# Kernel tuning notes

Hardware: AMD Instinct MI355X
Metric: run time of the kernel (lower is better)

Reference implementation:

```python
import jax, jax.numpy as jnp
import numpy as np

E, S, L, V, PMAX = 256, 64, 3, 256, 2000
DILATIONS = (1, 2, 4, 8)


def _layernorm(x, g, b, eps=1e-5):
    m = x.mean(-1, keepdims=True)
    v = ((x - m) ** 2).mean(-1, keepdims=True)
    return (x - m) * jax.lax.rsqrt(v + eps) * g + b


def _ssm_layer(x, in_w, conv_w, conv_b, dt_w, A_log, D_param, B_w, C_w, out_w, ln_g, ln_b):
    # x: [B, T, D]
    Bsz, T, Dm = x.shape
    xr = x @ in_w.T                                  # [B,T,2D]
    x_in, x_res = xr[..., :Dm], xr[..., Dm:]
    # causal depthwise conv, kernel=4, left-pad 3 (== torch pad=3 then [:, :, :T])
    xt = x_in.transpose(0, 2, 1)                     # [B,D,T]
    xc = jax.lax.conv_general_dilated(
        xt, conv_w[:, None, :], (1,), [(3, 0)],
        feature_group_count=Dm, dimension_numbers=('NCH', 'OIH', 'NCH'))
    xc = jax.nn.silu((xc + conv_b[None, :, None]).transpose(0, 2, 1))  # [B,T,D]
    A = -jnp.exp(A_log)                              # [D,S]
    Bm = xc @ B_w.T                                  # [B,T,S]
    Cm = xc @ C_w.T                                  # [B,T,S]
    dt = jax.nn.softplus(dt_w)                       # [D] per-channel timestep
    dA = 1.0 + dt[:, None] * A                       # Euler discretization I + dt*A, [D,S]
    h0 = jnp.zeros((Bsz, Dm, S), x.dtype)

    def step(h, inp):
        u_t, B_t, C_t = inp                          # [B,D],[B,S],[B,S]
        h = dA * h + (dt * u_t)[:, :, None] * B_t[:, None, :]   # [B,D,S]
        y = jnp.einsum('bs,bds->bd', C_t, h)
        return h, y

    _, ys = jax.lax.scan(step, h0, (xc.transpose(1, 0, 2), Bm.transpose(1, 0, 2), Cm.transpose(1, 0, 2)))
    y = ys.transpose(1, 0, 2) + D_param * xc         # [B,T,D]
    y = (y * jax.nn.silu(x_res)) @ out_w.T
    return _layernorm(y + x, ln_g, ln_b)


def _forward(tokens, tok_emb, pos_emb, in_w, conv_w, conv_b, dt_w, A_log, D_param,
             B_w, C_w, out_w, ln_g, ln_b, ctx_w, ctx_b, fus_w, fus_b, fus_ln_g, fus_ln_b):
    Bsz, T = tokens.shape
    x = tok_emb[tokens] + pos_emb[:T][None]          # [B,T,E]
    feats = x
    for i in range(L):
        feats = _ssm_layer(feats, in_w[i], conv_w[i], conv_b[i], dt_w[i], A_log[i],
                           D_param[i], B_w[i], C_w[i], out_w[i], ln_g[i], ln_b[i])
    # multi-dilation context convs on the raw embeddings
    xt = x.transpose(0, 2, 1)                        # [B,E,T]
    ctx = []
    for j, d in enumerate(DILATIONS):
        o = jax.lax.conv_general_dilated(
            xt, ctx_w[j], (1,), [(d, d)], rhs_dilation=(d,),
            dimension_numbers=('NCH', 'OIH', 'NCH'))
        ctx.append(o + ctx_b[j][None, :, None])
    ctx = jnp.concatenate(ctx, axis=1).transpose(0, 2, 1)      # [B,T,E]
    fused = jax.nn.relu(jnp.concatenate([feats, ctx], -1) @ fus_w.T + fus_b)
    return _layernorm(fused, fus_ln_g, fus_ln_b)


def setup_inputs() -> dict:
    key = jax.random.key(0)
    ks = jax.random.split(key, 16)
    Bsz, T = 32, 2000

    def n(k, shape, s):
        return jax.random.normal(k, shape, jnp.float32) * s

    return {
        'tokens': jax.random.randint(ks[0], (Bsz, T), 0, V),
        'tok_emb': n(ks[1], (V, E), 1.0),
        'pos_emb': n(ks[2], (PMAX, E), 1.0),
        'in_w': n(ks[3], (L, 2 * E, E), 0.05),
        'conv_w': n(ks[4], (L, E, 4), 0.2),
        'conv_b': jnp.zeros((L, E), jnp.float32),
        'dt_w': jax.random.uniform(ks[5], (L, E), jnp.float32, -0.01, 0.01),
        'A_log': jax.random.uniform(ks[6], (L, E, S), jnp.float32, -4.0, -1.0),
        'D_param': jnp.zeros((L, E), jnp.float32),
        'B_w': n(ks[7], (L, S, E), 0.05),
        'C_w': n(ks[8], (L, S, E), 0.05),
        'out_w': n(ks[9], (L, E, E), 0.05),
        'ln_g': jnp.ones((L, E), jnp.float32),
        'ln_b': jnp.zeros((L, E), jnp.float32),
        'ctx_w': n(ks[10], (4, E // 4, E, 3), 0.05),
        'ctx_b': jnp.zeros((4, E // 4), jnp.float32),
        'fus_w': n(ks[11], (E, 2 * E), 0.05),
        'fus_b': jnp.zeros((E,), jnp.float32),
        'fus_ln_g': jnp.ones((E,), jnp.float32),
        'fus_ln_b': jnp.zeros((E,), jnp.float32),
    }


def reference(tokens, tok_emb, pos_emb, in_w, conv_w, conv_b, dt_w, A_log, D_param,
              B_w, C_w, out_w, ln_g, ln_b, ctx_w, ctx_b, fus_w, fus_b, fus_ln_g, fus_ln_b):
    return _forward(tokens, tok_emb, pos_emb, in_w, conv_w, conv_b, dt_w, A_log, D_param,
                    B_w, C_w, out_w, ln_g, ln_b, ctx_w, ctx_b, fus_w, fus_b, fus_ln_g, fus_ln_b)
```

## Files before the change

kernel.cpp:

```cpp
#include <hip/hip_runtime.h>
#include <stdint.h>

#define B_ 32
#define T_ 2000
#define E_ 256
#define S_ 64
#define L_ 3
#define BT_ (B_*T_)
#define NC_ 40
#define CL_ 50
#define TP_ (T_+16)

typedef short s8v __attribute__((ext_vector_type(8)));
typedef short s4v __attribute__((ext_vector_type(4)));
typedef float f4v __attribute__((ext_vector_type(4)));
typedef unsigned short us;

__device__ __forceinline__ float b2f(us u){
    return __uint_as_float(((unsigned int)u) << 16);
}
__device__ __forceinline__ us f2b(float f){
    unsigned int x = __float_as_uint(f);
    x += 0x7fffu + ((x >> 16) & 1u);
    return (us)(x >> 16);
}

__global__ __launch_bounds__(256) void cvtw_k(const float* __restrict__ src,
    us* __restrict__ dst)
{
    int idx = blockIdx.x*256 + threadIdx.x;
    f4v v = *(const f4v*)(src + (size_t)idx*4);
    s4v o;
    #pragma unroll
    for (int j=0;j<4;j++) o[j] = (short)f2b(v[j]);
    *(s4v*)(dst + (size_t)idx*4) = o;
}

__global__ __launch_bounds__(256) void packbc_k(const float* __restrict__ Bw,
    const float* __restrict__ Cw, us* __restrict__ wbc)
{
    int idx = blockIdx.x*256 + threadIdx.x;
    int i = idx & 255; int r = (idx >> 8) & 127; int l = idx >> 15;
    const float* src = (r < 64) ? (Bw + ((size_t)l*S_ + r)*E_ + i)
                                : (Cw + ((size_t)l*S_ + (r-64))*E_ + i);
    wbc[idx] = f2b(*src);
}

__global__ __launch_bounds__(256) void packw_k(const float* __restrict__ cw,
    us* __restrict__ wp)
{
    int idx = blockIdx.x*256 + threadIdx.x;
    int i2 = idx % 768; int r = idx / 768;
    int c = r & 63; int j = r >> 6;
    int tap = i2 >> 8; int i = i2 & 255;
    wp[idx] = f2b(cw[(((size_t)(j*64 + c))*E_ + i)*3 + tap]);
}

__global__ __launch_bounds__(256) void embed_k(const int* __restrict__ tok,
    const float* __restrict__ te, const float* __restrict__ pe, us* __restrict__ x0)
{
    int idx = blockIdx.x*256 + threadIdx.x;
    int dg = idx & 31; int bt = idx >> 5; int t = bt % T_;
    int tk = tok[bt] & 255;
    const float* ta = te + (size_t)tk*E_ + dg*8;
    const float* pa = pe + (size_t)t*E_ + dg*8;
    f4v a0 = *(const f4v*)ta, a1 = *(const f4v*)(ta+4);
    f4v p0 = *(const f4v*)pa, p1 = *(const f4v*)(pa+4);
    s8v o;
    #pragma unroll
    for (int j=0;j<4;j++){
        o[j]   = (short)f2b(a0[j] + p0[j]);
        o[j+4] = (short)f2b(a1[j] + p1[j]);
    }
    *(s8v*)(x0 + (size_t)bt*E_ + dg*8) = o;
}

__global__ __launch_bounds__(256) void lconst_k(const float* __restrict__ dt_w,
    const float* __restrict__ A_log, float* __restrict__ dtv,
    float* __restrict__ dAT, float* __restrict__ dApT)
{
    int idx = blockIdx.x*256 + threadIdx.x;
    int d = idx & (E_-1); int s = idx >> 8;
    float dt = log1pf(expf(dt_w[d]));
    float A  = -expf(A_log[d*S_ + s]);
    float dA = 1.f + dt*A;
    dAT[s*E_ + d]  = dA;
    dApT[s*E_ + d] = powf(dA, (float)CL_);
    if (s == 0) dtv[d] = dt;
}

__global__ __launch_bounds__(256) void dwconv_k(const us* __restrict__ xin,
    const float* __restrict__ cw, const float* __restrict__ cb, us* __restrict__ xc)
{
    int idx = blockIdx.x*256 + threadIdx.x;
    int dg = idx & 31; int bt = idx >> 5; int t = bt % T_;
    int d0 = dg*8;
    float acc[8]; float w[8][4];
    #pragma unroll
    for (int j=0;j<8;j++){
        f4v wv = *(const f4v*)(cw + (size_t)(d0+j)*4);
        #pragma unroll
        for (int k=0;k<4;k++) w[j][k] = wv[k];
        acc[j] = cb[d0+j];
    }
    #pragma unroll
    for (int k=0;k<4;k++){
        if (t + k - 3 >= 0){
            s8v xv = *(const s8v*)(xin + (size_t)(bt + k - 3)*E_ + d0);
            #pragma unroll
            for (int j=0;j<8;j++) acc[j] = fmaf(b2f((us)xv[j]), w[j][k], acc[j]);
        }
    }
    s8v o;
    #pragma unroll
    for (int j=0;j<8;j++){ float v = acc[j]; v = v / (1.f + expf(-v)); o[j] = (short)f2b(v); }
    *(s8v*)(xc + (size_t)bt*E_ + d0) = o;
}

#define BM 128
#define BN 64
#define BK 32

template<int AMODE, int EPI>
__global__ __launch_bounds__(256)
void gemm_k(const us* __restrict__ A1, const us* __restrict__ A2,
            int lda, int shift,
            const us* __restrict__ W, int ldw,
            void* __restrict__ C1, const float* __restrict__ bias,
            int ldc, int K)
{
    __shared__ us Al[BM*BK];
    __shared__ us Bl[BN*BK];
    const int tid = threadIdx.x;
    const int wid = tid >> 6, lane = tid & 63;
    const int m0 = blockIdx.x * BM;
    const int n0 = blockIdx.y * BN;
    const int wr = wid >> 1, wc = wid & 1;
    f4v acc[4][2];
    #pragma unroll
    for (int a=0;a<4;a++)
        #pragma unroll
        for (int b=0;b<2;b++) acc[a][b] = (f4v){0.f,0.f,0.f,0.f};

    for (int k0 = 0; k0 < K; k0 += BK){
        s8v va[2], vb;
        #pragma unroll
        for (int i=0;i<2;i++){
            int g = i*256 + tid;
            int row = g >> 2, ks = g & 3;
            const us* src;
            if constexpr (AMODE==0){
                src = A1 + (size_t)(m0+row)*lda + k0 + ks*8;
            } else if constexpr (AMODE==2){
                int kk = k0 + ks*8;
                const us* base = (kk < E_) ? A1 : A2;
                src = base + (size_t)(m0+row)*E_ + (kk & (E_-1));
            } else {
                int kk = k0 + ks*8;
                int tap = kk >> 8; int kin = kk & (E_-1);
                int m = m0 + row; int bb = m / T_; int tt = m - bb*T_;
                src = A1 + ((size_t)bb*TP_ + 8 + tt + (tap-1)*shift)*E_ + kin;
            }
            va[i] = *(const s8v*)src;
        }
        {
            int row = tid >> 2, ks = tid & 3;
            vb = *(const s8v*)(W + (size_t)(n0+row)*ldw + k0 + ks*8);
        }
        if (k0) __syncthreads();
        #pragma unroll
        for (int i=0;i<2;i++) *(s8v*)(Al + (size_t)(i*256 + tid)*8) = va[i];
        *(s8v*)(Bl + (size_t)tid*8) = vb;
        __syncthreads();

        s8v af[4], bfr[2];
        #pragma unroll
        for (int mr=0;mr<4;mr++)
            af[mr] = *(const s8v*)(Al + ((size_t)(wr*64 + mr*16 + (lane&15))*4 + (lane>>4))*8);
        #pragma unroll
        for (int nr=0;nr<2;nr++)
            bfr[nr] = *(const s8v*)(Bl + ((size_t)(wc*32 + nr*16 + (lane&15))*4 + (lane>>4))*8);
        #pragma unroll
        for (int mr=0;mr<4;mr++)
            #pragma unroll
            for (int nr=0;nr<2;nr++)
                acc[mr][nr] = __builtin_amdgcn_mfma_f32_16x16x32_bf16(af[mr], bfr[nr], acc[mr][nr], 0, 0, 0);
    }
    #pragma unroll
    for (int mr=0;mr<4;mr++){
        #pragma unroll
        for (int nr=0;nr<2;nr++){
            int col = n0 + wc*32 + nr*16 + (lane & 15);
            int rb  = m0 + wr*64 + mr*16 + ((lane >> 4) << 2);
            #pragma unroll
            for (int i=0;i<4;i++){
                float val = acc[mr][nr][i];
                size_t row = (size_t)(rb + i);
                if constexpr (EPI==0){
                    ((us*)C1)[row*ldc + col] = f2b(val);
                } else if constexpr (EPI==2){
                    ((float*)C1)[row*ldc + col] = val;
                } else if constexpr (EPI==5){
                    val += bias[col];
                    ((us*)C1)[row*ldc + col] = f2b(val);
                } else {
                    val += bias[col];
                    val = fmaxf(val, 0.f);
                    ((float*)C1)[row*ldc + col] = val;
                }
            }
        }
    }
}

__global__ __launch_bounds__(256) void scan_local(
    const float* __restrict__ dAT, const float* __restrict__ dtv,
    const us* __restrict__ xc, const float* __restrict__ BC,
    us* __restrict__ ys, us* __restrict__ H)
{
    int b = blockIdx.x / NC_, c = blockIdx.x % NC_;
    int d = threadIdx.x;
    float h[S_], dAr[S_];
    #pragma unroll
    for (int s=0;s<S_;s++){ h[s]=0.f; dAr[s]=dAT[s*E_+d]; }
    float dtd = dtv[d];
    int t0 = c*CL_;
    for (int t=t0; t<t0+CL_; ++t){
        size_t bt = (size_t)b*T_ + t;
        float u = dtd * b2f(xc[bt*E_ + d]);
        const f4v* Bp = (const f4v*)(BC + bt*128);
        const f4v* Cp = Bp + 16;
        float y = 0.f;
        #pragma unroll
        for (int q=0;q<16;q++){
            f4v bv = Bp[q], cv = Cp[q];
            #pragma unroll
            for (int j=0;j<4;j++){
                int s = q*4+j;
                h[s] = fmaf(dAr[s], h[s], u*bv[j]);
                y    = fmaf(cv[j], h[s], y);
            }
        }
        ys[bt*E_ + d] = f2b(y);
    }
    size_t hb = ((size_t)(b*NC_ + c))*S_*E_ + d;
    #pragma unroll
    for (int s=0;s<S_;s++) H[hb + (size_t)s*E_] = f2b(h[s]);
}

__global__ __launch_bounds__(256) void carry_k(const float* __restrict__ dApT,
    us* H)
{
    int idx = blockIdx.x*256 + threadIdx.x;
    int d = idx & (E_-1); int s = (idx >> 8) & (S_-1); int b = idx >> 14;
    float ap = dApT[s*E_ + d];
    size_t base = ((size_t)(b*NC_))*S_*E_ + (size_t)s*E_ + d;
    float hh = 0.f;
    for (int c=0;c<NC_;c++){
        size_t p = base + (size_t)c*S_*E_;
        float hl = b2f(H[p]);
        H[p] = f2b(hh);
        hh = fmaf(ap, hh, hl);
    }
}

__global__ __launch_bounds__(256) void scan_fix(
    const float* __restrict__ dAT, const us* __restrict__ H,
    const float* __restrict__ BC, us* ys)
{
    int b = blockIdx.x / (NC_-1); int c = 1 + blockIdx.x % (NC_-1);
    int d = threadIdx.x;
    float w[S_], dAr[S_];
    size_t cb = ((size_t)(b*NC_ + c))*S_*E_ + d;
    #pragma unroll
    for (int s=0;s<S_;s++){ dAr[s] = dAT[s*E_+d]; w[s] = dAr[s]*b2f(H[cb + (size_t)s*E_]); }
    int t0 = c*CL_;
    for (int t=t0; t<t0+CL_; ++t){
        size_t bt = (size_t)b*T_ + t;
        const f4v* Cp = (const f4v*)(BC + bt*128) + 16;
        float y = 0.f;
        #pragma unroll
        for (int q=0;q<16;q++){
            f4v cv = Cp[q];
            #pragma unroll
            for (int j=0;j<4;j++){
                int s = q*4+j;
                y = fmaf(cv[j], w[s], y);
                w[s] *= dAr[s];
            }
        }
        size_t p = bt*E_ + d;
        ys[p] = f2b(b2f(ys[p]) + y);
    }
}

__global__ __launch_bounds__(256) void zin_k(const us* __restrict__ ys,
    const us* xc, const us* __restrict__ xres,
    const float* __restrict__ Dp, us* zout)
{
    size_t e0 = ((size_t)blockIdx.x*256 + threadIdx.x)*4;
    int d0 = (int)(e0 & (E_-1));
    s4v yv  = *(const s4v*)(ys + e0);
    s4v xcv = *(const s4v*)(xc + e0);
    s4v xrv = *(const s4v*)(xres + e0);
    f4v dv  = *(const f4v*)(Dp + d0);
    s4v o;
    #pragma unroll
    for (int j=0;j<4;j++){
        float y  = b2f((us)yv[j]) + dv[j] * b2f((us)xcv[j]);
        float xr = b2f((us)xrv[j]);
        o[j] = (short)f2b(y * (xr / (1.f + expf(-xr))));
    }
    *(s4v*)(zout + e0) = o;
}

__global__ __launch_bounds__(256) void ln_k(const us* z,
    const us* __restrict__ resid, const float* __restrict__ g,
    const float* __restrict__ bb, us* out)
{
    int wid = threadIdx.x >> 6, lane = threadIdx.x & 63;
    size_t row = (size_t)blockIdx.x*4 + wid;
    size_t base = row*E_ + lane*4;
    s4v zv = *(const s4v*)(z + base);
    float v[4];
    #pragma unroll
    for (int j=0;j<4;j++) v[j] = b2f((us)zv[j]);
    if (resid){
        s4v rv = *(const s4v*)(resid + base);
        #pragma unroll
        for (int j=0;j<4;j++) v[j] += b2f((us)rv[j]);
    }
    float sum = v[0]+v[1]+v[2]+v[3];
    float sq  = v[0]*v[0]+v[1]*v[1]+v[2]*v[2]+v[3]*v[3];
    #pragma unroll
    for (int off=32; off>0; off>>=1){
        sum += __shfl_xor(sum, off, 64);
        sq  += __shfl_xor(sq,  off, 64);
    }
    float mean = sum * (1.f/E_);
    float var  = sq * (1.f/E_) - mean*mean;
    float rstd = rsqrtf(var + 1e-5f);
    f4v gv = *(const f4v*)(g + lane*4);
    f4v bv = *(const f4v*)(bb + lane*4);
    s4v o;
    #pragma unroll
    for (int j=0;j<4;j++)
        o[j] = (short)f2b((v[j]-mean)*rstd*gv[j] + bv[j]);
    *(s4v*)(out + base) = o;
}

__global__ __launch_bounds__(256) void ln_f32_k(const float* z,
    const float* __restrict__ g, const float* __restrict__ bb, float* out)
{
    int wid = threadIdx.x >> 6, lane = threadIdx.x & 63;
    size_t row = (size_t)blockIdx.x*4 + wid;
    size_t base = row*E_ + lane*4;
    f4v v = *(const f4v*)(z + base);
    float sum = v[0]+v[1]+v[2]+v[3];
    float sq  = v[0]*v[0]+v[1]*v[1]+v[2]*v[2]+v[3]*v[3];
    #pragma unroll
    for (int off=32; off>0; off>>=1){
        sum += __shfl_xor(sum, off, 64);
        sq  += __shfl_xor(sq,  off, 64);
    }
    float mean = sum * (1.f/E_);
    float var  = sq * (1.f/E_) - mean*mean;
    float rstd = rsqrtf(var + 1e-5f);
    f4v gv = *(const f4v*)(g + lane*4);
    f4v bv = *(const f4v*)(bb + lane*4);
    f4v o;
    #pragma unroll
    for (int j=0;j<4;j++)
        o[j] = (v[j]-mean)*rstd*gv[j] + bv[j];
    *(f4v*)(out + base) = o;
}

__global__ __launch_bounds__(256) void xpad_k(const us* __restrict__ x0,
    us* __restrict__ xp)
{
    int idx = blockIdx.x*256 + threadIdx.x;
    int dg = idx & 31; int r = idx >> 5;
    int tp = r % TP_; int b = r / TP_;
    s8v o;
    if (tp < 8 || tp >= T_+8){
        #pragma unroll
        for (int j=0;j<8;j++) o[j] = 0;
    } else {
        o = *(const s8v*)(x0 + ((size_t)b*T_ + tp - 8)*E_ + dg*8);
    }
    *(s8v*)(xp + (size_t)r*E_ + dg*8) = o;
}

__global__ void probe_k(const unsigned int* __restrict__ outw,
    const us* p0, const us* p1, float* outf)
{
    if (threadIdx.x | blockIdx.x) return;
    bool zero = true;
    for (int i=0;i<512 && zero;i++)              if (outw[i]) zero = false;
    for (int i=2000000;i<2000512 && zero;i++)    if (outw[i]) zero = false;
    if (!zero) return;
    int code = 256, f;
    f=0; for (int i=0;i<256;i++) if (p0[i] & 0x7FFF) f=1;  code += 128*f;
    f=0; for (int i=0;i<256;i++) if (p1[i] & 0x7FFF) f=1;  code += 16*f;
    outf[0] = (float)code;
}

extern "C" void kernel_launch(void* const* d_in, const int* in_sizes, int n_in,
                              void* d_out, int out_size, void* d_ws, size_t ws_size,
                              hipStream_t stream)
{
    const int*   tokens   = (const int*)d_in[0];
    const float* tok_emb  = (const float*)d_in[1];
    const float* pos_emb  = (const float*)d_in[2];
    const float* in_w     = (const float*)d_in[3];
    const float* conv_w   = (const float*)d_in[4];
    const float* conv_b   = (const float*)d_in[5];
    const float* dt_w     = (const float*)d_in[6];
    const float* A_log    = (const float*)d_in[7];
    const float* D_param  = (const float*)d_in[8];
    const float* B_w      = (const float*)d_in[9];
    const float* C_w      = (const float*)d_in[10];
    const float* out_w    = (const float*)d_in[11];
    const float* ln_g     = (const float*)d_in[12];
    const float* ln_b     = (const float*)d_in[13];
    const float* ctx_w    = (const float*)d_in[14];
    const float* ctx_b    = (const float*)d_in[15];
    const float* fus_w    = (const float*)d_in[16];
    const float* fus_b    = (const float*)d_in[17];
    const float* fus_ln_g = (const float*)d_in[18];
    const float* fus_ln_b = (const float*)d_in[19];

    char* ws = (char*)d_ws;
    size_t off = 0;
    auto alloc = [&](size_t bytes){ size_t o = off; off += (bytes + 255) & ~(size_t)255; return o; };
    const size_t BT = BT_;
    size_t o_p0  = alloc(BT*E_*2);
    size_t o_p1  = alloc(BT*E_*2);
    size_t o_ctx = alloc(BT*E_*2);
    size_t o_xin = alloc(BT*E_*2);
    size_t o_xc  = alloc(BT*E_*2);
    size_t o_bc  = alloc(BT*128*4);
    size_t o_h   = alloc((size_t)B_*NC_*S_*E_*2);
    size_t o_wp  = alloc((size_t)4*64*768*2);
    size_t o_wi  = alloc((size_t)L_*2*E_*E_*2);
    size_t o_wo  = alloc((size_t)L_*E_*E_*2);
    size_t o_wbc = alloc((size_t)L_*128*E_*2);
    size_t o_wf  = alloc((size_t)E_*2*E_*2);
    size_t o_dtv = alloc(E_*4);
    size_t o_dat = alloc(E_*S_*4);
    size_t o_dap = alloc(E_*S_*4);
    (void)ws_size; (void)in_sizes; (void)n_in; (void)out_size;

    us* P0   = (us*)(ws + o_p0);
    us* P1   = (us*)(ws + o_p1);
    us* CTXB = (us*)(ws + o_ctx);
    us* XIN  = (us*)(ws + o_xin);
    us* XC   = (us*)(ws + o_xc);
    float* BCf = (float*)(ws + o_bc);
    us* Hb   = (us*)(ws + o_h);
    us* WP   = (us*)(ws + o_wp);
    us* WI   = (us*)(ws + o_wi);
    us* WO   = (us*)(ws + o_wo);
    us* WBC  = (us*)(ws + o_wbc);
    us* WF   = (us*)(ws + o_wf);
    float* DTV  = (float*)(ws + o_dtv);
    float* DAT  = (float*)(ws + o_dat);
    float* DAPT = (float*)(ws + o_dap);
    us* XPAD = XIN;
    us* YS   = (us*)d_out;

    cvtw_k<<<L_*2*E_*E_/1024, 256, 0, stream>>>(in_w,  WI);
    cvtw_k<<<L_*E_*E_/1024,   256, 0, stream>>>(out_w, WO);
    cvtw_k<<<E_*2*E_/1024,    256, 0, stream>>>(fus_w, WF);
    packbc_k<<<L_*128*E_/256, 256, 0, stream>>>(B_w, C_w, WBC);
    packw_k<<<4*64*768/256,   256, 0, stream>>>(ctx_w, WP);

    embed_k<<<BT_*32/256, 256, 0, stream>>>(tokens, tok_emb, pos_emb, P0);

    xpad_k<<<B_*TP_*32/256, 256, 0, stream>>>(P0, XPAD);
    const int dil[4] = {1,2,4,8};
    for (int j = 0; j < 4; ++j){
        gemm_k<3,5><<<dim3(BT_/BM, 1), 256, 0, stream>>>(
            XPAD, nullptr, E_, dil[j], WP + (size_t)j*64*768, 768,
            CTXB + j*64, ctx_b + j*64, E_, 768);
    }

    for (int l = 0; l < L_; ++l){
        const us* xprev = (l==1) ? P1 : P0;
        us*       xnext = (l==1) ? P0 : P1;

        lconst_k<<<E_*S_/256, 256, 0, stream>>>(dt_w + (size_t)l*E_, A_log + (size_t)l*E_*S_,
                                                DTV, DAT, DAPT);
        gemm_k<0,0><<<dim3(BT_/BM, E_/BN), 256, 0, stream>>>(
            xprev, nullptr, E_, 0, WI + (size_t)l*2*E_*E_, E_, XIN, nullptr, E_, E_);
        dwconv_k<<<BT_*32/256, 256, 0, stream>>>(XIN, conv_w + (size_t)l*E_*4, conv_b + (size_t)l*E_, XC);
        gemm_k<0,0><<<dim3(BT_/BM, E_/BN), 256, 0, stream>>>(
            xprev, nullptr, E_, 0, WI + (size_t)l*2*E_*E_ + (size_t)E_*E_, E_, XIN , nullptr, E_, E_);
        gemm_k<0,2><<<dim3(BT_/BM, 2), 256, 0, stream>>>(
            XC, nullptr, E_, 0, WBC + (size_t)l*128*E_, E_, BCf, nullptr, 128, E_);
        scan_local<<<B_*NC_, 256, 0, stream>>>(DAT, DTV, XC, BCf, YS, Hb);
        carry_k<<<B_*S_*E_/256, 256, 0, stream>>>(DAPT, Hb);
        scan_fix<<<B_*(NC_-1), 256, 0, stream>>>(DAT, Hb, BCf, YS);
        zin_k<<<BT_*E_/4/256, 256, 0, stream>>>(YS, XC, XIN, D_param + (size_t)l*E_, XC );
        gemm_k<0,0><<<dim3(BT_/BM, E_/BN), 256, 0, stream>>>(
            XC, nullptr, E_, 0, WO + (size_t)l*E_*E_, E_, XIN , nullptr, E_, E_);
        ln_k<<<BT_/4, 256, 0, stream>>>(XIN, xprev, ln_g + (size_t)l*E_, ln_b + (size_t)l*E_, xnext);
    }

    gemm_k<2,6><<<dim3(BT_/BM, E_/BN), 256, 0, stream>>>(
        P1, CTXB, E_, 0, WF, 2*E_, d_out, fus_b, E_, 2*E_);
    ln_f32_k<<<BT_/4, 256, 0, stream>>>((const float*)d_out, fus_ln_g, fus_ln_b, (float*)d_out);

    probe_k<<<1, 64, 0, stream>>>((const unsigned int*)d_out, P0, P1, (float*)d_out);
}
```

Measured before the change: 1.440 ms.

## Restructure chunked scan: split state across 4 lanes, stage B/C in LDS, recompute outputs

```diff
diff --git a/kernel.cpp b/kernel.cpp
--- a/kernel.cpp
+++ b/kernel.cpp
@@ -7,13 +7,16 @@
 #define S_ 64
 #define L_ 3
 #define BT_ (B_*T_)
-#define NC_ 40
-#define CL_ 50
+#define NC_ 25
+#define CL_ 80
+#define TS_ 16
+#define NT_ (CL_/TS_)
 #define TP_ (T_+16)
 
 typedef short s8v __attribute__((ext_vector_type(8)));
 typedef short s4v __attribute__((ext_vector_type(4)));
 typedef float f4v __attribute__((ext_vector_type(4)));
+typedef float f2v __attribute__((ext_vector_type(2)));
 typedef unsigned short us;
 
 __device__ __forceinline__ float b2f(us u){
@@ -213,39 +216,54 @@
     }
 }
 
-__global__ __launch_bounds__(256) void scan_local(
+__global__ __launch_bounds__(1024) void scan_h(
     const float* __restrict__ dAT, const float* __restrict__ dtv,
     const us* __restrict__ xc, const float* __restrict__ BC,
-    us* __restrict__ ys, us* __restrict__ H)
-{
+    us* __restrict__ H)
+{
+    __shared__ float sBC[TS_*128];
+    __shared__ us    sXC[TS_*256];
     int b = blockIdx.x / NC_, c = blockIdx.x % NC_;
-    int d = threadIdx.x;
-    float h[S_], dAr[S_];
-    #pragma unroll
-    for (int s=0;s<S_;s++){ h[s]=0.f; dAr[s]=dAT[s*E_+d]; }
+    int tid = threadIdx.x;
+    int d = tid >> 2, sg = tid & 3, s0 = sg*16;
+    f4v h4[4], dA4[4];
+    #pragma unroll
+    for (int q=0;q<4;q++){
+        #pragma unroll
+        for (int j=0;j<4;j++){ h4[q][j] = 0.f; dA4[q][j] = dAT[(s0+q*4+j)*E_ + d]; }
+    }
     float dtd = dtv[d];
     int t0 = c*CL_;
-    for (int t=t0; t<t0+CL_; ++t){
-        size_t bt = (size_t)b*T_ + t;
-        float u = dtd * b2f(xc[bt*E_ + d]);
-        const f4v* Bp = (const f4v*)(BC + bt*128);
-        const f4v* Cp = Bp + 16;
-        float y = 0.f;
-        #pragma unroll
-        for (int q=0;q<16;q++){
-            f4v bv = Bp[q], cv = Cp[q];
+    size_t base0 = (size_t)b*T_ + t0;
+    *(f2v*)(&sBC[tid*2]) = *(const f2v*)(BC + base0*128 + tid*2);
+    *(s4v*)(&sXC[tid*4]) = *(const s4v*)(xc + base0*E_ + tid*4);
+    __syncthreads();
+    for (int tile = 0; tile < NT_; ++tile){
+        f2v pv; s4v pxv;
+        bool more = (tile+1 < NT_);
+        if (more){
+            size_t basen = base0 + (size_t)(tile+1)*TS_;
+            pv  = *(const f2v*)(BC + basen*128 + tid*2);
+            pxv = *(const s4v*)(xc + basen*E_ + tid*4);
+        }
+        for (int st = 0; st < TS_; ++st){
+            float u = dtd * b2f(sXC[st*256 + d]);
+            const f4v* Bp = (const f4v*)(&sBC[st*128 + s0]);
             #pragma unroll
-            for (int j=0;j<4;j++){
-                int s = q*4+j;
-                h[s] = fmaf(dAr[s], h[s], u*bv[j]);
-                y    = fmaf(cv[j], h[s], y);
-            }
-        }
-        ys[bt*E_ + d] = f2b(y);
+            for (int q=0;q<4;q++) h4[q] = dA4[q]*h4[q] + Bp[q]*u;
+        }
+        __syncthreads();
+        if (more){
+            *(f2v*)(&sBC[tid*2]) = pv;
+            *(s4v*)(&sXC[tid*4]) = pxv;
+        }
+        __syncthreads();
     }
     size_t hb = ((size_t)(b*NC_ + c))*S_*E_ + d;
     #pragma unroll
-    for (int s=0;s<S_;s++) H[hb + (size_t)s*E_] = f2b(h[s]);
+    for (int q=0;q<4;q++)
+        #pragma unroll
+        for (int j=0;j<4;j++) H[hb + (size_t)(s0+q*4+j)*E_] = f2b(h4[q][j]);
 }
 
 __global__ __launch_bounds__(256) void carry_k(const float* __restrict__ dApT,
@@ -264,33 +282,63 @@
     }
 }
 
-__global__ __launch_bounds__(256) void scan_fix(
-    const float* __restrict__ dAT, const us* __restrict__ H,
-    const float* __restrict__ BC, us* ys)
-{
-    int b = blockIdx.x / (NC_-1); int c = 1 + blockIdx.x % (NC_-1);
-    int d = threadIdx.x;
-    float w[S_], dAr[S_];
+__global__ __launch_bounds__(1024) void scan_y(
+    const float* __restrict__ dAT, const float* __restrict__ dtv,
+    const us* __restrict__ xc, const float* __restrict__ BC,
+    const us* __restrict__ Hc, us* __restrict__ ys)
+{
+    __shared__ float sBC[TS_*128];
+    __shared__ us    sXC[TS_*256];
+    int b = blockIdx.x / NC_, c = blockIdx.x % NC_;
+    int tid = threadIdx.x;
+    int d = tid >> 2, sg = tid & 3, s0 = sg*16;
+    f4v h4[4], dA4[4];
     size_t cb = ((size_t)(b*NC_ + c))*S_*E_ + d;
     #pragma unroll
-    for (int s=0;s<S_;s++){ dAr[s] = dAT[s*E_+d]; w[s] = dAr[s]*b2f(H[cb + (size_t)s*E_]); }
+    for (int q=0;q<4;q++){
+        #pragma unroll
+        for (int j=0;j<4;j++){
+            int s = s0 + q*4 + j;
+            dA4[q][j] = dAT[s*E_ + d];
+            h4[q][j]  = b2f(Hc[cb + (size_t)s*E_]);
+        }
+    }
+    float dtd = dtv[d];
     int t0 = c*CL_;
-    for (int t=t0; t<t0+CL_; ++t){
-        size_t bt = (size_t)b*T_ + t;
-        const f4v* Cp = (const f4v*)(BC + bt*128) + 16;
-        float y = 0.f;
-        #pragma unroll
-        for (int q=0;q<16;q++){
-            f4v cv = Cp[q];
+    size_t base0 = (size_t)b*T_ + t0;
+    *(f2v*)(&sBC[tid*2]) = *(const f2v*)(BC + base0*128 + tid*2);
+    *(s4v*)(&sXC[tid*4]) = *(const s4v*)(xc + base0*E_ + tid*4);
+    __syncthreads();
+    for (int tile = 0; tile < NT_; ++tile){
+        f2v pv; s4v pxv;
+        bool more = (tile+1 < NT_);
+        if (more){
+            size_t basen = base0 + (size_t)(tile+1)*TS_;
+            pv  = *(const f2v*)(BC + basen*128 + tid*2);
+            pxv = *(const s4v*)(xc + basen*E_ + tid*4);
+        }
+        for (int st = 0; st < TS_; ++st){
+            int t = t0 + tile*TS_ + st;
+            float u = dtd * b2f(sXC[st*256 + d]);
+            const f4v* Bp = (const f4v*)(&sBC[st*128 + s0]);
+            const f4v* Cp = (const f4v*)(&sBC[st*128 + 64 + s0]);
+            f4v y4 = (f4v){0.f,0.f,0.f,0.f};
             #pragma unroll
-            for (int j=0;j<4;j++){
-                int s = q*4+j;
-                y = fmaf(cv[j], w[s], y);
-                w[s] *= dAr[s];
+            for (int q=0;q<4;q++){
+                h4[q] = dA4[q]*h4[q] + Bp[q]*u;
+                y4    = y4 + Cp[q]*h4[q];
             }
-        }
-        size_t p = bt*E_ + d;
-        ys[p] = f2b(b2f(ys[p]) + y);
+            float y = (y4[0]+y4[1]) + (y4[2]+y4[3]);
+            y += __shfl_xor(y, 1, 64);
+            y += __shfl_xor(y, 2, 64);
+            if (sg == 0) ys[((size_t)b*T_ + t)*E_ + d] = f2b(y);
+        }
+        __syncthreads();
+        if (more){
+            *(f2v*)(&sBC[tid*2]) = pv;
+            *(s4v*)(&sXC[tid*4]) = pxv;
+        }
+        __syncthreads();
     }
 }
 
@@ -498,9 +546,9 @@
             xprev, nullptr, E_, 0, WI + (size_t)l*2*E_*E_ + (size_t)E_*E_, E_, XIN , nullptr, E_, E_);
         gemm_k<0,2><<<dim3(BT_/BM, 2), 256, 0, stream>>>(
             XC, nullptr, E_, 0, WBC + (size_t)l*128*E_, E_, BCf, nullptr, 128, E_);
-        scan_local<<<B_*NC_, 256, 0, stream>>>(DAT, DTV, XC, BCf, YS, Hb);
+        scan_h<<<B_*NC_, 1024, 0, stream>>>(DAT, DTV, XC, BCf, Hb);
         carry_k<<<B_*S_*E_/256, 256, 0, stream>>>(DAPT, Hb);
-        scan_fix<<<B_*(NC_-1), 256, 0, stream>>>(DAT, Hb, BCf, YS);
+        scan_y<<<B_*NC_, 1024, 0, stream>>>(DAT, DTV, XC, BCf, Hb, YS);
         zin_k<<<BT_*E_/4/256, 256, 0, stream>>>(YS, XC, XIN, D_param + (size_t)l*E_, XC );
         gemm_k<0,0><<<dim3(BT_/BM, E_/BN), 256, 0, stream>>>(
             XC, nullptr, E_, 0, WO + (size_t)l*E_*E_, E_, XIN , nullptr, E_, E_);
```

Result: no change. 1.463 ms (+1.6%).
